# Optimization experiments

Measured on AMD Instinct MI355X. Metric: run time of the kernel, lower is better.

The kernel has to match this reference:

```python
import jax, jax.numpy as jnp
import numpy as np

B, T, C, H = 2, 2048, 1024, 16
HD = C // H  # 64
EPS = 1e-5


def _layernorm(x, g, b):
    mu = jnp.mean(x, axis=-1, keepdims=True)
    var = jnp.mean(jnp.square(x - mu), axis=-1, keepdims=True)
    return (x - mu) * jax.lax.rsqrt(var + EPS) * g + b


def setup_inputs() -> dict:
    key = jax.random.key(0)
    ks = jax.random.split(key, 12)
    s = 0.02
    return {
        "x": jax.random.normal(ks[0], (B, T, C), dtype=jnp.float32),
        # per-head q/k/v projections stacked over heads: [H, C, HD]
        "Wq": jax.random.normal(ks[1], (H, C, HD), dtype=jnp.float32) * s,
        "Wk": jax.random.normal(ks[2], (H, C, HD), dtype=jnp.float32) * s,
        "Wv": jax.random.normal(ks[3], (H, C, HD), dtype=jnp.float32) * s,
        "Wp": jax.random.normal(ks[4], (C, C), dtype=jnp.float32) * s,
        "bp": jnp.zeros((C,), dtype=jnp.float32),
        "W1": jax.random.normal(ks[5], (C, 4 * C), dtype=jnp.float32) * s,
        "b1": jnp.zeros((4 * C,), dtype=jnp.float32),
        "W2": jax.random.normal(ks[6], (4 * C, C), dtype=jnp.float32) * s,
        "b2": jnp.zeros((C,), dtype=jnp.float32),
        "g1": jnp.ones((C,), dtype=jnp.float32),
        "be1": jnp.zeros((C,), dtype=jnp.float32),
        "g2": jnp.ones((C,), dtype=jnp.float32),
        "be2": jnp.zeros((C,), dtype=jnp.float32),
    }


def reference(x, Wq, Wk, Wv, Wp, bp, W1, b1, W2, b2, g1, be1, g2, be2):
    b, t, c = x.shape
    hd = Wq.shape[-1]
    # multi-head causal self-attention (heads vectorized instead of Python loop)
    q = jnp.einsum('btc,hcd->bhtd', x, Wq)
    k = jnp.einsum('btc,hcd->bhtd', x, Wk)
    v = jnp.einsum('btc,hcd->bhtd', x, Wv)
    scores = jnp.einsum('bhtd,bhsd->bhts', q, k) * (float(hd) ** -0.5)
    causal = jnp.tril(jnp.ones((t, t), dtype=bool))
    scores = jnp.where(causal, scores, -jnp.inf)
    probs = jax.nn.softmax(scores, axis=-1)  # dropout is identity in eval
    o = jnp.einsum('bhts,bhsd->bhtd', probs, v)
    o = o.transpose(0, 2, 1, 3).reshape(b, t, c)  # concat heads
    attn_out = o @ Wp + bp
    # residual + post-norm
    x = _layernorm(x + attn_out, g1, be1)
    # FFN (dropout identity in eval)
    ff = jax.nn.relu(x @ W1 + b1) @ W2 + b2
    x = _layernorm(x + ff, g2, be2)
    return x
```

## Files before the change

### kernel.cpp

```cpp
#include <hip/hip_runtime.h>
#include <cstdint>
#include <cstddef>

typedef __attribute__((ext_vector_type(8))) short short8;
typedef __attribute__((ext_vector_type(4))) short short4v;
typedef __attribute__((ext_vector_type(4))) float f32x4;
typedef __attribute__((ext_vector_type(2))) uint32_t u32x2;

#define Bdim 2
#define Tdim 2048
#define Cdim 1024
#define Hdim 16
#define HDdim 64
#define Mdim (Bdim*Tdim)
#define FFdim (4*Cdim)

__device__ __forceinline__ uint16_t f2bf(float f) {
    union { float f; uint32_t u; } v; v.f = f;
    uint32_t x = v.u;
    uint32_t r = x + 0x7FFFu + ((x >> 16) & 1u);
    return (uint16_t)(r >> 16);
}
__device__ __forceinline__ float bf2f(uint16_t h) {
    union { float f; uint32_t u; } v; v.u = ((uint32_t)h) << 16; return v.f;
}
__device__ __forceinline__ uint32_t cvtpk(float lo, float hi) {
    uint32_t r;
    asm("v_cvt_pk_bf16_f32 %0, %1, %2" : "=v"(r) : "v"(lo), "v"(hi));
    return r;
}

__device__ __forceinline__ void gload_lds16(const uint16_t* g, uint16_t* l) {
    __builtin_amdgcn_global_load_lds(
        (const __attribute__((address_space(1))) void*)g,
        (__attribute__((address_space(3))) void*)l, 16, 0, 0);
}

#define RAW_BAR()   asm volatile("s_barrier" ::: "memory")
#define VMCNT(N)    asm volatile("s_waitcnt vmcnt(" #N ")" ::: "memory")
#define LGKM0()     asm volatile("s_waitcnt lgkmcnt(0)" ::: "memory")

__global__ __launch_bounds__(256) void prep_k(const float* __restrict__ x,
                                              uint16_t* __restrict__ xb,
                                              const float* __restrict__ Wq,
                                              const float* __restrict__ Wk,
                                              const float* __restrict__ Wv,
                                              uint16_t* __restrict__ wqkv,
                                              const float* __restrict__ Wp,
                                              uint16_t* __restrict__ wpt,
                                              const float* __restrict__ W1,
                                              uint16_t* __restrict__ w1t,
                                              const float* __restrict__ W2,
                                              uint16_t* __restrict__ w2t) {
    const int id = blockIdx.x, tid = threadIdx.x;
    if (id < 4096) {
        int i = id * 1024 + tid * 4;
        f32x4 v = *(const f32x4*)(x + i);
        short4v o;
#pragma unroll
        for (int j = 0; j < 4; ++j) o[j] = (short)f2bf(v[j]);
        *(short4v*)(xb + i) = o;
        return;
    }
    __shared__ uint16_t tile[32][33];
    const float* in; uint16_t* out; int R, Cc, bx, by;
    if (id < 7168) {
        int r = id - 4096, w = r >> 10, idx = r & 1023;
        int bz = idx >> 6;
        bx = idx & 31; by = (idx >> 5) & 1;
        R = 1024; Cc = 64;
        in  = (w == 0 ? Wq : w == 1 ? Wk : Wv) + (size_t)bz * 65536;
        out = wqkv + (size_t)w * 1048576 + (size_t)bz * 65536;
    } else if (id < 8192) {
        int idx = id - 7168;
        bx = idx & 31; by = idx >> 5;
        R = 1024; Cc = 1024; in = Wp; out = wpt;
    } else if (id < 12288) {
        int idx = id - 8192;
        bx = idx & 31; by = idx >> 5;
        R = 1024; Cc = 4096; in = W1; out = w1t;
    } else {
        int idx = id - 12288;
        bx = idx & 127; by = idx >> 7;
        R = 4096; Cc = 1024; in = W2; out = w2t;
    }
    const int r0 = bx * 32, n0 = by * 32;
    const int tx = tid & 31, ty = tid >> 5;
#pragma unroll
    for (int i = 0; i < 4; ++i) {
        int r = ty + 8 * i;
        tile[r][tx] = f2bf(in[(size_t)(r0 + r) * Cc + n0 + tx]);
    }
    __syncthreads();
#pragma unroll
    for (int i = 0; i < 4; ++i) {
        int n = ty + 8 * i;
        out[(size_t)(n0 + n) * R + r0 + tx] = tile[tx][n];
    }
}

__global__ __launch_bounds__(256) void vtrans_k(const uint16_t* __restrict__ qkv,
                                                uint16_t* __restrict__ vT) {
    __shared__ uint16_t tile[32][33];
    const int bh = blockIdx.z, b = bh >> 4, h = bh & 15;
    const uint16_t* vp = qkv + (size_t)b * Tdim * (3 * Cdim) + 2 * Cdim + h * HDdim;
    uint16_t* op = vT + (size_t)bh * HDdim * Tdim;
    const int t0 = blockIdx.x * 32, d0 = blockIdx.y * 32;
    const int tx = threadIdx.x, ty = threadIdx.y;
#pragma unroll
    for (int i = 0; i < 4; ++i) {
        int r = ty + 8 * i;
        tile[r][tx] = vp[(size_t)(t0 + r) * (3 * Cdim) + d0 + tx];
    }
    __syncthreads();
    const int tp = t0 + (((tx >> 2) & 3) << 3) + (((tx >> 4) & 1) << 2) + (tx & 3);
#pragma unroll
    for (int i = 0; i < 4; ++i) {
        int d = ty + 8 * i;
        op[(size_t)(d0 + d) * Tdim + tp] = tile[tx][d];
    }
}

template<bool BIAS, bool RELU, int RES, bool OUTF>
__global__ __launch_bounds__(512, 4) void gemm128_k(const uint16_t* __restrict__ A,
                                                    const uint16_t* __restrict__ Bt,
                                                    int Kfull, int Kp,
                                                    float* outF,
                                                    uint16_t* __restrict__ outB,
                                                    const float* __restrict__ bias,
                                                    const float* __restrict__ residF,
                                                    const uint16_t* __restrict__ residB,
                                                    uint16_t* __restrict__ outP1,
                                                    uint16_t* __restrict__ outP2,
                                                    uint16_t* __restrict__ outP3,
                                                    int N) {
    __shared__ uint16_t lds[32768];
    const int bx = blockIdx.x, by = blockIdx.y, kz = blockIdx.z;
    const int tid = threadIdx.x;
    const int wave = tid >> 6, lane = tid & 63;
    const int lg = lane >> 4, lr = lane & 15, lr7 = lr & 7;
    const int wm = wave >> 2, wn = wave & 3;
    const int NT = Kp >> 6;

    const int aOff = wm * 4096 + lr * 64;
    const int bOff = 16384 + wn * 2048 + lr * 64;
    const int g0 = 8 * (lg ^ lr7);
    const int g1 = 8 * ((4 + lg) ^ lr7);

    const int srow = tid >> 3;
    const int scol = 8 * ((tid & 7) ^ (srow & 7));
    const uint16_t* aSrc = A + (size_t)(bx * 128 + srow) * Kfull + (size_t)kz * Kp + scol;
    const uint16_t* bSrc = Bt + (size_t)(by * 128 + srow) * Kfull + (size_t)kz * Kp + scol;
    const size_t r64 = (size_t)64 * Kfull;

#define STG_A(pp, tt) do {                                                        \
        _Pragma("unroll")                                                         \
        for (int h_ = 0; h_ < 2; ++h_)                                            \
            gload_lds16(aSrc + h_ * r64 + (size_t)(tt) * 64,                      \
                        &lds[(pp) * 8192 + h_ * 4096 + wave * 512]);              \
    } while (0)
#define STG_B(pp, tt) do {                                                        \
        _Pragma("unroll")                                                         \
        for (int h_ = 0; h_ < 2; ++h_)                                            \
            gload_lds16(bSrc + h_ * r64 + (size_t)(tt) * 64,                      \
                        &lds[16384 + (pp) * 8192 + h_ * 4096 + wave * 512]);      \
    } while (0)
#define MM(M, Nn, AF, BF) acc[M][Nn] = __builtin_amdgcn_mfma_f32_16x16x32_bf16(AF, BF, acc[M][Nn], 0, 0, 0)

    f32x4 acc[4][2];
#pragma unroll
    for (int i = 0; i < 4; ++i)
#pragma unroll
        for (int j = 0; j < 2; ++j) acc[i][j] = (f32x4){0.f, 0.f, 0.f, 0.f};

    STG_B(0, 0); STG_A(0, 0);
    if (NT > 1) { STG_B(1, 1); STG_A(1, 1); VMCNT(4); }
    else VMCNT(0);
    RAW_BAR();

    for (int t = 0; t < NT; ++t) {
        const int p = t & 1, p13 = p << 13;
        const bool nx1 = (t + 1 < NT), nx2 = (t + 2 < NT);
        short8 a0[4], b0[2], a1[4], b1[2];

#pragma unroll
        for (int m = 0; m < 4; ++m) a0[m] = *(const short8*)&lds[p13 + aOff + 1024 * m + g0];
#pragma unroll
        for (int nn = 0; nn < 2; ++nn) b0[nn] = *(const short8*)&lds[p13 + bOff + 1024 * nn + g0];
        __builtin_amdgcn_s_setprio(1);
#pragma unroll
        for (int m = 0; m < 4; ++m)
#pragma unroll
            for (int nn = 0; nn < 2; ++nn) MM(m, nn, a0[m], b0[nn]);
        __builtin_amdgcn_s_setprio(0);

#pragma unroll
        for (int m = 0; m < 4; ++m) a1[m] = *(const short8*)&lds[p13 + aOff + 1024 * m + g1];
#pragma unroll
        for (int nn = 0; nn < 2; ++nn) b1[nn] = *(const short8*)&lds[p13 + bOff + 1024 * nn + g1];
        __builtin_amdgcn_s_setprio(1);
#pragma unroll
        for (int m = 0; m < 4; ++m)
#pragma unroll
            for (int nn = 0; nn < 2; ++nn) MM(m, nn, a1[m], b1[nn]);
        __builtin_amdgcn_s_setprio(0);

        LGKM0();
        RAW_BAR();
        if (nx2) { STG_B(p, t + 2); STG_A(p, t + 2); }
        if (nx1) {
            if (nx2) VMCNT(4); else VMCNT(0);
            RAW_BAR();
        }
    }
#undef STG_A
#undef STG_B
#undef MM
    if (kz == 0) {
#pragma unroll
        for (int nn = 0; nn < 2; ++nn) {
            const int col = (by << 7) + wn * 32 + 16 * nn + lr;
            const float bv = BIAS ? bias[col] : 0.f;
#pragma unroll
            for (int m = 0; m < 4; ++m) {
#pragma unroll
                for (int r = 0; r < 4; ++r) {
                    const int row = (bx << 7) + wm * 64 + 16 * m + 4 * lg + r;
                    float v = acc[m][nn][r] + bv;
                    if (RELU) v = fmaxf(v, 0.f);
                    if (RES == 1) v += residF[(size_t)row * N + col];
                    if (RES == 2) v += bf2f(residB[(size_t)row * N + col]);
                    if (OUTF) outF[(size_t)row * N + col] = v;
                    else      outB[(size_t)row * N + col] = f2bf(v);
                }
            }
        }
    } else {
        uint16_t* op = (kz == 1) ? outP1 : (kz == 2) ? outP2 : outP3;
#pragma unroll
        for (int nn = 0; nn < 2; ++nn) {
            const int col = (by << 7) + wn * 32 + 16 * nn + lr;
#pragma unroll
            for (int m = 0; m < 4; ++m) {
#pragma unroll
                for (int r = 0; r < 4; ++r) {
                    const int row = (bx << 7) + wm * 64 + 16 * m + 4 * lg + r;
                    op[(size_t)row * N + col] = f2bf(acc[m][nn][r]);
                }
            }
        }
    }
}

__global__ __launch_bounds__(256) void attn_k(const uint16_t* __restrict__ qkv,
                                              const uint16_t* __restrict__ vT,
                                              uint16_t* __restrict__ o) {
    __shared__ uint16_t Kb[2][64 * 64];
    __shared__ uint16_t Vb[2][64 * 64];
    const int tid = threadIdx.x;
    const int wave = tid >> 6, lane = tid & 63;
    const int lg = lane >> 4, lr = lane & 15, lr7 = lr & 7;
    const int bh = blockIdx.x, b = bh >> 4, h = bh & 15;
    const int yy = blockIdx.y, k4 = yy >> 3, y0 = yy & 7;
    const int tx = (k4 == 0) ? y0 : (k4 == 1) ? 31 - y0 : (k4 == 2) ? 8 + y0 : 23 - y0;
    const size_t rs = 3 * Cdim;
    const uint16_t* qp = qkv + (size_t)b * Tdim * rs + (size_t)h * HDdim;
    const uint16_t* kp = qp + Cdim;
    const uint16_t* vtp = vT + (size_t)bh * HDdim * Tdim;

    const int s0 = tid, s1 = tid + 256;
    const int r0v = s0 >> 3, c0v = ((s0 & 7) ^ (r0v & 7)) << 3;
    const int r1v = s1 >> 3, c1v = ((s1 & 7) ^ (r1v & 7)) << 3;
    const int db0 = wave * 512, db1 = 2048 + wave * 512;

    const int q0 = tx << 6;
    const int nch = tx + 1;
    const int qrow = q0 + 16 * wave + lr;

    const uint16_t* kp0 = kp + (size_t)r0v * rs + c0v;
    const uint16_t* kp1 = kp + (size_t)r1v * rs + c1v;
    const uint16_t* vt0 = vtp + (size_t)r0v * Tdim + c0v;
    const uint16_t* vt1 = vtp + (size_t)r1v * Tdim + c1v;
    const size_t kstep = (size_t)64 * rs;

#define STAGE(bufi)                                  \
    do {                                             \
        gload_lds16(kp0, &Kb[bufi][db0]);            \
        gload_lds16(kp1, &Kb[bufi][db1]);            \
        gload_lds16(vt0, &Vb[bufi][db0]);            \
        gload_lds16(vt1, &Vb[bufi][db1]);            \
    } while (0)

    short8 qf[2];
#pragma unroll
    for (int c = 0; c < 2; ++c) {
        short8 raw = *(const short8*)(qp + (size_t)qrow * rs + 32 * c + 8 * lg);
#pragma unroll
        for (int j = 0; j < 8; ++j)
            qf[c][j] = (short)f2bf(bf2f((uint16_t)raw[j]) * 0.18033688f);
    }

    f32x4 l4 = (f32x4){0.f, 0.f, 0.f, 0.f};
    f32x4 oacc[4];
#pragma unroll
    for (int t = 0; t < 4; ++t) oacc[t] = (f32x4){0.f, 0.f, 0.f, 0.f};

    STAGE(0);
    kp0 += kstep; kp1 += kstep; vt0 += 64; vt1 += 64;
    __syncthreads();
    int cur = 0;
    for (int ch = 0; ch < nch; ++ch) {
        if (ch + 1 < nch) {
            STAGE(cur ^ 1);
            kp0 += kstep; kp1 += kstep; vt0 += 64; vt1 += 64;
        }
        const int kvb = 64 * ch;
        const char* Kc = (const char*)&Kb[cur][0];
        const char* Vc = (const char*)&Vb[cur][0];
        short8 kf[4][2];
#pragma unroll
        for (int u = 0; u < 4; ++u)
#pragma unroll
            for (int c = 0; c < 2; ++c)
                kf[u][c] = *(const short8*)(Kc + (16 * u + lr) * 128 +
                                            (((lg + 4 * c) ^ lr7) << 4));
        f32x4 s4[4];
        __builtin_amdgcn_s_setprio(1);
#pragma unroll
        for (int u = 0; u < 4; ++u) {
            f32x4 z = (f32x4){0.f, 0.f, 0.f, 0.f};
            z = __builtin_amdgcn_mfma_f32_16x16x32_bf16(kf[u][0], qf[0], z, 0, 0, 0);
            z = __builtin_amdgcn_mfma_f32_16x16x32_bf16(kf[u][1], qf[1], z, 0, 0, 0);
            s4[u] = z;
        }
        __builtin_amdgcn_s_setprio(0);
        if (ch + 1 == nch) {
#pragma unroll
            for (int u = 0; u < 4; ++u)
#pragma unroll
                for (int r = 0; r < 4; ++r) {
                    int kv = kvb + 16 * u + 4 * lg + r;
                    if (kv > qrow) s4[u][r] = -__builtin_inff();
                }
        }
        float p[4][4];
#pragma unroll
        for (int u = 0; u < 4; ++u)
#pragma unroll
            for (int r = 0; r < 4; ++r) {
                float e = exp2f(s4[u][r] - 16.f);
                p[u][r] = e; l4[r] += e;
            }
        short8 pb[2];
#pragma unroll
        for (int hh = 0; hh < 2; ++hh) {
            union { uint32_t w[4]; short8 v; } q_;
            q_.w[0] = cvtpk(p[2 * hh][0], p[2 * hh][1]);
            q_.w[1] = cvtpk(p[2 * hh][2], p[2 * hh][3]);
            q_.w[2] = cvtpk(p[2 * hh + 1][0], p[2 * hh + 1][1]);
            q_.w[3] = cvtpk(p[2 * hh + 1][2], p[2 * hh + 1][3]);
            pb[hh] = q_.v;
        }
        __builtin_amdgcn_s_setprio(1);
#pragma unroll
        for (int t = 0; t < 4; ++t) {
            const int vbase = (16 * t + lr) * 128;
            f32x4 oa = oacc[t];
#pragma unroll
            for (int hh = 0; hh < 2; ++hh) {
                short8 vf = *(const short8*)(Vc + vbase + (((4 * hh + lg) ^ lr7) << 4));
                oa = __builtin_amdgcn_mfma_f32_16x16x32_bf16(vf, pb[hh], oa, 0, 0, 0);
            }
            oacc[t] = oa;
        }
        __builtin_amdgcn_s_setprio(0);
        __syncthreads();
        cur ^= 1;
    }
    float l = (l4[0] + l4[1]) + (l4[2] + l4[3]);
    l += __shfl_xor(l, 16);
    l += __shfl_xor(l, 32);
    const float inv = 1.f / l;
    uint16_t* orow = o + (size_t)(b * Tdim + qrow) * Cdim + h * HDdim;
#pragma unroll
    for (int t = 0; t < 4; ++t) {
        u32x2 wv;
        wv[0] = cvtpk(oacc[t][0] * inv, oacc[t][1] * inv);
        wv[1] = cvtpk(oacc[t][2] * inv, oacc[t][3] * inv);
        *(u32x2*)(orow + 16 * t + 4 * lg) = wv;
    }
#undef STAGE
}

__global__ __launch_bounds__(256) void ln_k(const float* __restrict__ in,
                                            const uint16_t* __restrict__ in2b,
                                            const float* __restrict__ g,
                                            const float* __restrict__ be,
                                            float* __restrict__ outF,
                                            uint16_t* __restrict__ outB) {
    const int row = blockIdx.x, tid = threadIdx.x;
    const size_t base = (size_t)row * Cdim + tid * 4;
    f32x4 xv = *(const f32x4*)(in + base);
    if (in2b) {
        short4v yv = *(const short4v*)(in2b + base);
#pragma unroll
        for (int j = 0; j < 4; ++j) xv[j] += bf2f((uint16_t)yv[j]);
    }
    float s = xv[0] + xv[1] + xv[2] + xv[3];
    float q = xv[0] * xv[0] + xv[1] * xv[1] + xv[2] * xv[2] + xv[3] * xv[3];
#pragma unroll
    for (int off = 1; off < 64; off <<= 1) { s += __shfl_xor(s, off); q += __shfl_xor(q, off); }
    __shared__ float sm[4], sq[4];
    if ((tid & 63) == 0) { sm[tid >> 6] = s; sq[tid >> 6] = q; }
    __syncthreads();
    s = sm[0] + sm[1] + sm[2] + sm[3];
    q = sq[0] + sq[1] + sq[2] + sq[3];
    const float mu = s * (1.f / 1024.f);
    const float var = q * (1.f / 1024.f) - mu * mu;
    const float rstd = rsqrtf(var + 1e-5f);
#pragma unroll
    for (int j = 0; j < 4; ++j) {
        int col = tid * 4 + j;
        float y = (xv[j] - mu) * rstd * g[col] + be[col];
        if (outF) outF[(size_t)row * Cdim + col] = y;
        if (outB) outB[(size_t)row * Cdim + col] = f2bf(y);
    }
}

__global__ __launch_bounds__(256) void lnp_k(const float* __restrict__ in,
                                             const uint16_t* __restrict__ p2,
                                             const uint16_t* __restrict__ p3,
                                             const uint16_t* __restrict__ p4,
                                             const float* __restrict__ g,
                                             const float* __restrict__ be,
                                             float* __restrict__ outF) {
    const int row = blockIdx.x, tid = threadIdx.x;
    const size_t base = (size_t)row * Cdim + tid * 4;
    f32x4 xv = *(const f32x4*)(in + base);
    short4v a2 = *(const short4v*)(p2 + base);
    short4v a3 = *(const short4v*)(p3 + base);
    short4v a4 = *(const short4v*)(p4 + base);
#pragma unroll
    for (int j = 0; j < 4; ++j)
        xv[j] += bf2f((uint16_t)a2[j]) + bf2f((uint16_t)a3[j]) + bf2f((uint16_t)a4[j]);
    float s = xv[0] + xv[1] + xv[2] + xv[3];
    float q = xv[0] * xv[0] + xv[1] * xv[1] + xv[2] * xv[2] + xv[3] * xv[3];
#pragma unroll
    for (int off = 1; off < 64; off <<= 1) { s += __shfl_xor(s, off); q += __shfl_xor(q, off); }
    __shared__ float sm[4], sq[4];
    if ((tid & 63) == 0) { sm[tid >> 6] = s; sq[tid >> 6] = q; }
    __syncthreads();
    s = sm[0] + sm[1] + sm[2] + sm[3];
    q = sq[0] + sq[1] + sq[2] + sq[3];
    const float mu = s * (1.f / 1024.f);
    const float var = q * (1.f / 1024.f) - mu * mu;
    const float rstd = rsqrtf(var + 1e-5f);
#pragma unroll
    for (int j = 0; j < 4; ++j) {
        int col = tid * 4 + j;
        outF[(size_t)row * Cdim + col] = (xv[j] - mu) * rstd * g[col] + be[col];
    }
}

extern "C" void kernel_launch(void* const* d_in, const int* in_sizes, int n_in,
                              void* d_out, int out_size, void* d_ws, size_t ws_size,
                              hipStream_t stream) {
    const float* x   = (const float*)d_in[0];
    const float* Wq  = (const float*)d_in[1];
    const float* Wk  = (const float*)d_in[2];
    const float* Wv  = (const float*)d_in[3];
    const float* Wp  = (const float*)d_in[4];
    const float* bp  = (const float*)d_in[5];
    const float* W1  = (const float*)d_in[6];
    const float* b1  = (const float*)d_in[7];
    const float* W2  = (const float*)d_in[8];
    const float* b2  = (const float*)d_in[9];
    const float* g1  = (const float*)d_in[10];
    const float* be1 = (const float*)d_in[11];
    const float* g2  = (const float*)d_in[12];
    const float* be2 = (const float*)d_in[13];
    float* out = (float*)d_out;

    char* ws = (char*)d_ws;
    uint16_t* qkv   = (uint16_t*)(ws + 0);
    uint16_t* P1p   = (uint16_t*)(ws + 0);
    uint16_t* h1    = (uint16_t*)(ws + 0);
    uint16_t* obuf  = (uint16_t*)(ws + 25165824);
    uint16_t* xb    = (uint16_t*)(ws + 33554432);
    uint16_t* vT    = (uint16_t*)(ws + 33554432);
    uint16_t* Q2    = (uint16_t*)(ws + 33554432);
    uint16_t* wqkv  = (uint16_t*)(ws + 41943040);
    uint16_t* x1b   = (uint16_t*)(ws + 41943040);
    uint16_t* wpt   = (uint16_t*)(ws + 48234496);
    float*    resid = (float*)   (ws + 50331648);
    uint16_t* Q1    = (uint16_t*)(ws + 50331648);
    float*    y0    = (float*)   (ws + 67108864);
    uint16_t* w1t   = (uint16_t*)(ws + 83886080);
    uint16_t* w2t   = (uint16_t*)(ws + 92274688);
    uint16_t* Q3    = (uint16_t*)(ws + 100663296);

    prep_k<<<16384, 256, 0, stream>>>(x, xb, Wq, Wk, Wv, wqkv, Wp, wpt, W1, w1t, W2, w2t);

    gemm128_k<false, false, 0, false><<<dim3(32, 24, 1), 512, 0, stream>>>(
        xb, wqkv, Cdim, Cdim, nullptr, qkv, nullptr, nullptr, nullptr,
        nullptr, nullptr, nullptr, 3 * Cdim);
    vtrans_k<<<dim3(64, 2, 32), dim3(32, 8), 0, stream>>>(qkv, vT);
    attn_k<<<dim3(32, 32), 256, 0, stream>>>(qkv, vT, obuf);
    gemm128_k<true, false, 1, true><<<dim3(32, 8, 2), 512, 0, stream>>>(
        obuf, wpt, Cdim, Cdim / 2, resid, nullptr, bp, x, nullptr,
        P1p, nullptr, nullptr, Cdim);
    ln_k<<<Mdim, 256, 0, stream>>>(resid, P1p, g1, be1, nullptr, x1b);
    gemm128_k<true, true, 0, false><<<dim3(32, 32, 1), 512, 0, stream>>>(
        x1b, w1t, Cdim, Cdim, nullptr, h1, b1, nullptr, nullptr,
        nullptr, nullptr, nullptr, FFdim);
    gemm128_k<true, false, 2, true><<<dim3(32, 8, 4), 512, 0, stream>>>(
        h1, w2t, FFdim, FFdim / 4, y0, nullptr, b2, nullptr, x1b,
        Q1, Q2, Q3, Cdim);
    lnp_k<<<Mdim, 256, 0, stream>>>(y0, Q1, Q2, Q3, g2, be2, out);
}
```

Baseline: 220.5 us.

## Fuse V transpose into QKV GEMM epilogue and compute softmax sum via MFMA

The QKV projection GEMM now writes V tiles directly in the transposed, permuted layout that attention expects, so the separate vtrans kernel launch and its extra read/write pass over V go away. The vT buffer moves to a workspace region that does not overlap xb. In attention, the per-lane row-sum accumulation and its cross-lane shuffles are replaced by an MFMA against a ones vector. This adds two MFMAs per chunk and sums the bf16-rounded probabilities, which shifts the normaliser slightly.

```diff
diff --git a/kernel.cpp b/kernel.cpp
--- a/kernel.cpp
+++ b/kernel.cpp
@@ -99,28 +99,6 @@
     }
 }
 
-__global__ __launch_bounds__(256) void vtrans_k(const uint16_t* __restrict__ qkv,
-                                                uint16_t* __restrict__ vT) {
-    __shared__ uint16_t tile[32][33];
-    const int bh = blockIdx.z, b = bh >> 4, h = bh & 15;
-    const uint16_t* vp = qkv + (size_t)b * Tdim * (3 * Cdim) + 2 * Cdim + h * HDdim;
-    uint16_t* op = vT + (size_t)bh * HDdim * Tdim;
-    const int t0 = blockIdx.x * 32, d0 = blockIdx.y * 32;
-    const int tx = threadIdx.x, ty = threadIdx.y;
-#pragma unroll
-    for (int i = 0; i < 4; ++i) {
-        int r = ty + 8 * i;
-        tile[r][tx] = vp[(size_t)(t0 + r) * (3 * Cdim) + d0 + tx];
-    }
-    __syncthreads();
-    const int tp = t0 + (((tx >> 2) & 3) << 3) + (((tx >> 4) & 1) << 2) + (tx & 3);
-#pragma unroll
-    for (int i = 0; i < 4; ++i) {
-        int d = ty + 8 * i;
-        op[(size_t)(d0 + d) * Tdim + tp] = tile[tx][d];
-    }
-}
-
 template<bool BIAS, bool RELU, int RES, bool OUTF>
 __global__ __launch_bounds__(512, 4) void gemm128_k(const uint16_t* __restrict__ A,
                                                     const uint16_t* __restrict__ Bt,
@@ -133,6 +111,8 @@
                                                     uint16_t* __restrict__ outP1,
                                                     uint16_t* __restrict__ outP2,
                                                     uint16_t* __restrict__ outP3,
+                                                    uint16_t* __restrict__ vOut,
+                                                    int byV,
                                                     int N) {
     __shared__ uint16_t lds[32768];
     const int bx = blockIdx.x, by = blockIdx.y, kz = blockIdx.z;
@@ -217,21 +197,40 @@
 #undef STG_B
 #undef MM
     if (kz == 0) {
-#pragma unroll
-        for (int nn = 0; nn < 2; ++nn) {
-            const int col = (by << 7) + wn * 32 + 16 * nn + lr;
-            const float bv = BIAS ? bias[col] : 0.f;
-#pragma unroll
-            for (int m = 0; m < 4; ++m) {
-#pragma unroll
-                for (int r = 0; r < 4; ++r) {
-                    const int row = (bx << 7) + wm * 64 + 16 * m + 4 * lg + r;
-                    float v = acc[m][nn][r] + bv;
-                    if (RELU) v = fmaxf(v, 0.f);
-                    if (RES == 1) v += residF[(size_t)row * N + col];
-                    if (RES == 2) v += bf2f(residB[(size_t)row * N + col]);
-                    if (OUTF) outF[(size_t)row * N + col] = v;
-                    else      outB[(size_t)row * N + col] = f2bf(v);
+        if (vOut != nullptr && by >= byV) {
+            const int bb = bx >> 4;
+            const int trow = (bx & 15) * 128 + wm * 64;
+#pragma unroll
+            for (int nn = 0; nn < 2; ++nn) {
+                const int ch = ((by - byV) << 7) + wn * 32 + 16 * nn + lr;
+                const int hh = ch >> 6, d = ch & 63;
+                uint16_t* vbase = vOut + ((size_t)(bb * 16 + hh) * 64 + d) * 2048;
+#pragma unroll
+                for (int m = 0; m < 4; ++m) {
+                    const int tp = trow + 32 * (m >> 1) + 8 * lg + 4 * (m & 1);
+                    short4v ov;
+#pragma unroll
+                    for (int r = 0; r < 4; ++r) ov[r] = (short)f2bf(acc[m][nn][r]);
+                    *(short4v*)(vbase + tp) = ov;
+                }
+            }
+        } else {
+#pragma unroll
+            for (int nn = 0; nn < 2; ++nn) {
+                const int col = (by << 7) + wn * 32 + 16 * nn + lr;
+                const float bv = BIAS ? bias[col] : 0.f;
+#pragma unroll
+                for (int m = 0; m < 4; ++m) {
+#pragma unroll
+                    for (int r = 0; r < 4; ++r) {
+                        const int row = (bx << 7) + wm * 64 + 16 * m + 4 * lg + r;
+                        float v = acc[m][nn][r] + bv;
+                        if (RELU) v = fmaxf(v, 0.f);
+                        if (RES == 1) v += residF[(size_t)row * N + col];
+                        if (RES == 2) v += bf2f(residB[(size_t)row * N + col]);
+                        if (OUTF) outF[(size_t)row * N + col] = v;
+                        else      outB[(size_t)row * N + col] = f2bf(v);
+                    }
                 }
             }
         }
@@ -299,8 +298,11 @@
         for (int j = 0; j < 8; ++j)
             qf[c][j] = (short)f2bf(bf2f((uint16_t)raw[j]) * 0.18033688f);
     }
-
-    f32x4 l4 = (f32x4){0.f, 0.f, 0.f, 0.f};
+    short8 ones;
+#pragma unroll
+    for (int j = 0; j < 8; ++j) ones[j] = (short)0x3F80;
+
+    f32x4 lacc = (f32x4){0.f, 0.f, 0.f, 0.f};
     f32x4 oacc[4];
 #pragma unroll
     for (int t = 0; t < 4; ++t) oacc[t] = (f32x4){0.f, 0.f, 0.f, 0.f};
@@ -347,10 +349,8 @@
 #pragma unroll
         for (int u = 0; u < 4; ++u)
 #pragma unroll
-            for (int r = 0; r < 4; ++r) {
-                float e = exp2f(s4[u][r] - 16.f);
-                p[u][r] = e; l4[r] += e;
-            }
+            for (int r = 0; r < 4; ++r)
+                p[u][r] = exp2f(s4[u][r] - 16.f);
         short8 pb[2];
 #pragma unroll
         for (int hh = 0; hh < 2; ++hh) {
@@ -362,6 +362,8 @@
             pb[hh] = q_.v;
         }
         __builtin_amdgcn_s_setprio(1);
+        lacc = __builtin_amdgcn_mfma_f32_16x16x32_bf16(ones, pb[0], lacc, 0, 0, 0);
+        lacc = __builtin_amdgcn_mfma_f32_16x16x32_bf16(ones, pb[1], lacc, 0, 0, 0);
 #pragma unroll
         for (int t = 0; t < 4; ++t) {
             const int vbase = (16 * t + lr) * 128;
@@ -377,10 +379,7 @@
         __syncthreads();
         cur ^= 1;
     }
-    float l = (l4[0] + l4[1]) + (l4[2] + l4[3]);
-    l += __shfl_xor(l, 16);
-    l += __shfl_xor(l, 32);
-    const float inv = 1.f / l;
+    const float inv = 1.f / lacc[0];
     uint16_t* orow = o + (size_t)(b * Tdim + qrow) * Cdim + h * HDdim;
 #pragma unroll
     for (int t = 0; t < 4; ++t) {
@@ -487,11 +486,11 @@
     uint16_t* h1    = (uint16_t*)(ws + 0);
     uint16_t* obuf  = (uint16_t*)(ws + 25165824);
     uint16_t* xb    = (uint16_t*)(ws + 33554432);
-    uint16_t* vT    = (uint16_t*)(ws + 33554432);
     uint16_t* Q2    = (uint16_t*)(ws + 33554432);
     uint16_t* wqkv  = (uint16_t*)(ws + 41943040);
     uint16_t* x1b   = (uint16_t*)(ws + 41943040);
     uint16_t* wpt   = (uint16_t*)(ws + 48234496);
+    uint16_t* vT    = (uint16_t*)(ws + 50331648);
     float*    resid = (float*)   (ws + 50331648);
     uint16_t* Q1    = (uint16_t*)(ws + 50331648);
     float*    y0    = (float*)   (ws + 67108864);
@@ -503,18 +502,17 @@
 
     gemm128_k<false, false, 0, false><<<dim3(32, 24, 1), 512, 0, stream>>>(
         xb, wqkv, Cdim, Cdim, nullptr, qkv, nullptr, nullptr, nullptr,
-        nullptr, nullptr, nullptr, 3 * Cdim);
-    vtrans_k<<<dim3(64, 2, 32), dim3(32, 8), 0, stream>>>(qkv, vT);
+        nullptr, nullptr, nullptr, vT, 16, 3 * Cdim);
     attn_k<<<dim3(32, 32), 256, 0, stream>>>(qkv, vT, obuf);
     gemm128_k<true, false, 1, true><<<dim3(32, 8, 2), 512, 0, stream>>>(
         obuf, wpt, Cdim, Cdim / 2, resid, nullptr, bp, x, nullptr,
-        P1p, nullptr, nullptr, Cdim);
+        P1p, nullptr, nullptr, nullptr, 1 << 30, Cdim);
     ln_k<<<Mdim, 256, 0, stream>>>(resid, P1p, g1, be1, nullptr, x1b);
     gemm128_k<true, true, 0, false><<<dim3(32, 32, 1), 512, 0, stream>>>(
         x1b, w1t, Cdim, Cdim, nullptr, h1, b1, nullptr, nullptr,
-        nullptr, nullptr, nullptr, FFdim);
+        nullptr, nullptr, nullptr, nullptr, 1 << 30, FFdim);
     gemm128_k<true, false, 2, true><<<dim3(32, 8, 4), 512, 0, stream>>>(
         h1, w2t, FFdim, FFdim / 4, y0, nullptr, b2, nullptr, x1b,
-        Q1, Q2, Q3, Cdim);
+        Q1, Q2, Q3, nullptr, 1 << 30, Cdim);
     lnp_k<<<Mdim, 256, 0, stream>>>(y0, Q1, Q2, Q3, g2, be2, out);
 }
```

Result: no change. 216.6 us (-1.8%).
